# Performance work log

Hardware: AMD Instinct MI355X
Metric: run time of the kernel (lower is better)

The kernel has to match this reference:

```python
import jax, jax.numpy as jnp
import numpy as np

B, S, D = 32, 1024, 128
NUM_VT = 32
MIN_DR, MAX_DR = 0.0, 30.0
MIN_SOG, MAX_SOG = 0.0, 40.0
MIN_ROT, MAX_ROT = -127.0, 127.0


def setup_inputs() -> dict:
    key = jax.random.key(0)
    ks = jax.random.split(key, 32)
    u = lambda k, lo, hi: jax.random.uniform(k, (B, S, 1), minval=lo, maxval=hi, dtype=jnp.float32)
    lon = u(ks[0], -180.0, 180.0)
    lat = u(ks[1], -90.0, 90.0)
    rot = u(ks[2], MIN_ROT, MAX_ROT)
    sog = u(ks[3], MIN_SOG, MAX_SOG)
    cog = u(ks[4], 0.0, 360.0)
    head = u(ks[5], 0.0, 360.0)
    vtype = jax.random.randint(ks[6], (B, S, 1), 0, NUM_VT).astype(jnp.float32)
    dr = u(ks[7], MIN_DR, MAX_DR)
    ais_data = jnp.concatenate([lon, lat, rot, sog, cog, head, vtype, dr], axis=-1)
    p = lambda k, shape: (jax.random.normal(k, shape, dtype=jnp.float32) * 0.05)
    return {
        "ais_data": ais_data,
        "W_lon1": p(ks[8], (2, D)), "b_lon1": p(ks[9], (D,)),
        "W_lon2": p(ks[10], (D, D)), "b_lon2": p(ks[11], (D,)),
        "W_lat1": p(ks[12], (2, D)), "b_lat1": p(ks[13], (D,)),
        "W_lat2": p(ks[14], (D, D)), "b_lat2": p(ks[15], (D,)),
        "W_cog": p(ks[16], (2, D)), "b_cog": p(ks[17], (D,)),
        "W_head": p(ks[18], (2, D)), "b_head": p(ks[19], (D,)),
        "W_dr": p(ks[20], (1, D)), "b_dr": p(ks[21], (D,)),
        "W_sog": p(ks[22], (1, D)), "b_sog": p(ks[23], (D,)),
        "W_rot": p(ks[24], (1, D)), "b_rot": p(ks[25], (D,)),
        "emb": p(ks[26], (NUM_VT, D)),
    }


def reference(ais_data, W_lon1, b_lon1, W_lon2, b_lon2, W_lat1, b_lat1, W_lat2, b_lat2,
              W_cog, b_cog, W_head, b_head, W_dr, b_dr, W_sog, b_sog, W_rot, b_rot, emb):
    deg2rad = jnp.pi / 180.0
    lon = ais_data[..., 0:1]
    lat = ais_data[..., 1:2]
    rot = ais_data[..., 2:3]
    sog = ais_data[..., 3:4]
    cog = ais_data[..., 4:5]
    head = ais_data[..., 5:6]
    vtype = ais_data[..., 6]
    dr = ais_data[..., 7:8]

    def coord(x, mask_val, W1, b1, W2, b2):
        # x: [b,s,1] degrees -> 2-layer MLP on [sin, cos]
        xr = x * deg2rad
        f = jnp.concatenate([jnp.sin(xr), jnp.cos(xr)], axis=-1)  # [b,s,2]
        e = jax.nn.relu(f @ W1 + b1) @ W2 + b2                    # [b,s,D]
        return jnp.where(x == mask_val, 0.0, e)

    def cyclical(x, W, b):
        xr = x * deg2rad - jnp.pi
        f = jnp.concatenate([jnp.sin(xr), jnp.cos(xr)], axis=-1)
        e = f @ W + b
        return jnp.where(x == -1.0, 0.0, e)

    def continuous(x, mn, mx, W, b):
        xn = 2.0 * (x - mn) / jnp.maximum(mx - mn, 1e-6) - 1.0
        e = jnp.tanh(xn @ W + b)
        return jnp.where(x == -1.0, 0.0, e)

    enc_lon = coord(lon, 181.0, W_lon1, b_lon1, W_lon2, b_lon2)
    enc_lat = coord(lat, 91.0, W_lat1, b_lat1, W_lat2, b_lat2)
    enc_rot = continuous(rot, MIN_ROT, MAX_ROT, W_rot, b_rot)
    enc_sog = continuous(sog, MIN_SOG, MAX_SOG, W_sog, b_sog)
    enc_cog = cyclical(cog, W_cog, b_cog)
    enc_head = cyclical(head, W_head, b_head)
    vt_idx = jax.lax.stop_gradient(vtype).astype(jnp.int32)
    enc_vt = emb[vt_idx]                                          # [b,s,D]
    enc_dr = continuous(dr, MIN_DR, MAX_DR, W_dr, b_dr)

    # order matches torch.cat((spatial(lon,lat), rot, sog, cog, heading, vessel_type, draught))
    out = jnp.stack([enc_lon, enc_lat, enc_rot, enc_sog, enc_cog, enc_head, enc_vt, enc_dr], axis=2)
    b, s = ais_data.shape[:2]
    return out.reshape(b, s, -1)  # [b, s, 8*D]
```

## Files before the change

kernel.cpp:

```cpp
#include <hip/hip_runtime.h>
#include <cstdint>

typedef short bf16x8 __attribute__((ext_vector_type(8)));
typedef float f32x4 __attribute__((ext_vector_type(4)));

#define D2R 0.017453292519943295f
#define PI_F 3.14159265358979323846f

__device__ __forceinline__ unsigned bf16r(float x) {
    unsigned u = __float_as_uint(x);
    return (u + 0x7fffu + ((u >> 16) & 1u)) >> 16;
}

__device__ __forceinline__ float tanh_fast(float x) {
    float e = __expf(2.0f * x);
    return 1.0f - 2.0f / (e + 1.0f);
}

__global__ __launch_bounds__(256, 2) void hae_kernel(
    const float* __restrict__ ais,
    const float* __restrict__ Wlon1, const float* __restrict__ blon1,
    const float* __restrict__ Wlon2, const float* __restrict__ blon2,
    const float* __restrict__ Wlat1, const float* __restrict__ blat1,
    const float* __restrict__ Wlat2, const float* __restrict__ blat2,
    const float* __restrict__ Wcog,  const float* __restrict__ bcog,
    const float* __restrict__ Whead, const float* __restrict__ bhead,
    const float* __restrict__ Wdr,   const float* __restrict__ bdr,
    const float* __restrict__ Wsog,  const float* __restrict__ bsog,
    const float* __restrict__ Wrot,  const float* __restrict__ brot,
    const float* __restrict__ emb,
    float* __restrict__ out)
{
    __shared__ unsigned short hlds[2][64][128];
    __shared__ float s_sin[2][64], s_cos[2][64], s_mask[2][64];
    __shared__ float s_xn[3][64], s_mxn[3][64];
    __shared__ float s_scyc[2][64], s_ccyc[2][64], s_mcyc[2][64];
    __shared__ int   s_vt[64];

    const int t = threadIdx.x;
    const int tok0 = blockIdx.x * 64;

    if (t < 64) {
        const float* a = ais + (size_t)(tok0 + t) * 8;
        f32x4 a0 = *(const f32x4*)a;
        f32x4 a1 = *(const f32x4*)(a + 4);
        float lon = a0[0], lat = a0[1], rot = a0[2], sog = a0[3];
        float cog = a1[0], head = a1[1], vt = a1[2], dr = a1[3];

        float lr = lon * D2R;
        s_sin[0][t] = __sinf(lr); s_cos[0][t] = __cosf(lr);
        s_mask[0][t] = (lon == 181.0f) ? 0.f : 1.f;
        float tr = lat * D2R;
        s_sin[1][t] = __sinf(tr); s_cos[1][t] = __cosf(tr);
        s_mask[1][t] = (lat == 91.0f) ? 0.f : 1.f;

        s_xn[0][t] = (rot + 127.0f) * (2.0f / 254.0f) - 1.0f;
        s_mxn[0][t] = (rot == -1.0f) ? 0.f : 1.f;
        s_xn[1][t] = sog * (2.0f / 40.0f) - 1.0f;
        s_mxn[1][t] = (sog == -1.0f) ? 0.f : 1.f;
        s_xn[2][t] = dr * (2.0f / 30.0f) - 1.0f;
        s_mxn[2][t] = (dr == -1.0f) ? 0.f : 1.f;

        float cr = cog * D2R - PI_F;
        s_scyc[0][t] = __sinf(cr); s_ccyc[0][t] = __cosf(cr);
        s_mcyc[0][t] = (cog == -1.0f) ? 0.f : 1.f;
        float hr = head * D2R - PI_F;
        s_scyc[1][t] = __sinf(hr); s_ccyc[1][t] = __cosf(hr);
        s_mcyc[1][t] = (head == -1.0f) ? 0.f : 1.f;
        s_vt[t] = (int)vt;
    }
    __syncthreads();

    {
        const int jj = t & 63;
        const int j0 = jj * 2;
        const int quad = t >> 6;
        float w00a = Wlon1[j0],       w00b = Wlon1[j0 + 1];
        float w01a = Wlon1[128 + j0], w01b = Wlon1[128 + j0 + 1];
        float b0a  = blon1[j0],       b0b  = blon1[j0 + 1];
        float w10a = Wlat1[j0],       w10b = Wlat1[j0 + 1];
        float w11a = Wlat1[128 + j0], w11b = Wlat1[128 + j0 + 1];
        float b1a  = blat1[j0],       b1b  = blat1[j0 + 1];
        char* base0 = (char*)&hlds[0][0][0];
        char* base1 = (char*)&hlds[1][0][0];
        #pragma unroll
        for (int p = 0; p < 16; ++p) {
            int i = quad + p * 4;
            int sw = (j0 * 2) ^ ((i & 7) << 4);
            float s0 = s_sin[0][i], c0 = s_cos[0][i];
            float h0 = fmaxf(fmaf(s0, w00a, fmaf(c0, w01a, b0a)), 0.f);
            float h1 = fmaxf(fmaf(s0, w00b, fmaf(c0, w01b, b0b)), 0.f);
            *(unsigned*)(base0 + i * 256 + sw) = bf16r(h0) | (bf16r(h1) << 16);
            float s1 = s_sin[1][i], c1 = s_cos[1][i];
            float g0 = fmaxf(fmaf(s1, w10a, fmaf(c1, w11a, b1a)), 0.f);
            float g1 = fmaxf(fmaf(s1, w10b, fmaf(c1, w11b, b1b)), 0.f);
            *(unsigned*)(base1 + i * 256 + sw) = bf16r(g0) | (bf16r(g1) << 16);
        }
    }
    __syncthreads();

    const int w  = t >> 6;
    const int l  = t & 63;
    const int c  = w & 1;
    const int mh = w >> 1;
    const float* W2 = c ? Wlat2 : Wlon2;
    const float* b2 = c ? blat2 : blon2;
    const int col = l & 15;
    const int q   = l >> 4;

    bf16x8 afrag[2][4];
    {
        char* hb = (char*)&hlds[c][0][0];
        #pragma unroll
        for (int mt = 0; mt < 2; ++mt) {
            int row = mh * 32 + mt * 16 + col;
            #pragma unroll
            for (int ks = 0; ks < 4; ++ks) {
                int jb = (ks * 32 + q * 8) * 2;
                afrag[mt][ks] = *(bf16x8*)(hb + row * 256 + (jb ^ ((row & 7) << 4)));
            }
        }
    }

    f32x4 acc[2][8];
    #pragma unroll
    for (int mt = 0; mt < 2; ++mt)
        #pragma unroll
        for (int nt = 0; nt < 8; ++nt)
            acc[mt][nt] = (f32x4){0.f, 0.f, 0.f, 0.f};

    #pragma unroll
    for (int nt = 0; nt < 8; ++nt) {
        const int d = nt * 16 + col;
        bf16x8 bfrag[4];
        #pragma unroll
        for (int ks = 0; ks < 4; ++ks) {
            int kb = ks * 32 + q * 8;
            bf16x8 bf;
            #pragma unroll
            for (int e = 0; e < 8; ++e)
                bf[e] = (short)bf16r(W2[(size_t)(kb + e) * 128 + d]);
            bfrag[ks] = bf;
        }
        #pragma unroll
        for (int mt = 0; mt < 2; ++mt)
            #pragma unroll
            for (int ks = 0; ks < 4; ++ks)
                acc[mt][nt] = __builtin_amdgcn_mfma_f32_16x16x32_bf16(
                    afrag[mt][ks], bfrag[ks], acc[mt][nt], 0, 0, 0);
    }

    #pragma unroll
    for (int nt = 0; nt < 8; ++nt) {
        int d = nt * 16 + col;
        float bb = b2[d];
        #pragma unroll
        for (int mt = 0; mt < 2; ++mt) {
            int tokb = mh * 32 + mt * 16 + q * 4;
            #pragma unroll
            for (int r = 0; r < 4; ++r) {
                int tl = tokb + r;
                float v = (acc[mt][nt][r] + bb) * s_mask[c][tl];
                out[(size_t)(tok0 + tl) * 1024 + c * 128 + d] = v;
            }
        }
    }

    {
        const int d4 = (t & 31) * 4;
        const int io = t >> 5;
        f32x4 wr  = *(const f32x4*)(Wrot + d4),        br_ = *(const f32x4*)(brot + d4);
        f32x4 wsg = *(const f32x4*)(Wsog + d4),        bs_ = *(const f32x4*)(bsog + d4);
        f32x4 wdd = *(const f32x4*)(Wdr + d4),         bd_ = *(const f32x4*)(bdr + d4);
        f32x4 wc0 = *(const f32x4*)(Wcog + d4),  wc1 = *(const f32x4*)(Wcog + 128 + d4),  bc_ = *(const f32x4*)(bcog + d4);
        f32x4 wh0 = *(const f32x4*)(Whead + d4), wh1 = *(const f32x4*)(Whead + 128 + d4), bh_ = *(const f32x4*)(bhead + d4);
        #pragma unroll
        for (int p = 0; p < 8; ++p) {
            int i = io + p * 8;
            float* ob = out + (size_t)(tok0 + i) * 1024;
            {
                float xn = s_xn[0][i], mk = s_mxn[0][i];
                f32x4 v;
                #pragma unroll
                for (int e = 0; e < 4; ++e) v[e] = tanh_fast(fmaf(xn, wr[e], br_[e])) * mk;
                *(f32x4*)(ob + 2 * 128 + d4) = v;
            }
            {
                float xn = s_xn[1][i], mk = s_mxn[1][i];
                f32x4 v;
                #pragma unroll
                for (int e = 0; e < 4; ++e) v[e] = tanh_fast(fmaf(xn, wsg[e], bs_[e])) * mk;
                *(f32x4*)(ob + 3 * 128 + d4) = v;
            }
            {
                float sc = s_scyc[0][i], cc = s_ccyc[0][i], mk = s_mcyc[0][i];
                f32x4 v;
                #pragma unroll
                for (int e = 0; e < 4; ++e) v[e] = fmaf(sc, wc0[e], fmaf(cc, wc1[e], bc_[e])) * mk;
                *(f32x4*)(ob + 4 * 128 + d4) = v;
            }
            {
                float sc = s_scyc[1][i], cc = s_ccyc[1][i], mk = s_mcyc[1][i];
                f32x4 v;
                #pragma unroll
                for (int e = 0; e < 4; ++e) v[e] = fmaf(sc, wh0[e], fmaf(cc, wh1[e], bh_[e])) * mk;
                *(f32x4*)(ob + 5 * 128 + d4) = v;
            }
            {
                f32x4 ev = *(const f32x4*)(emb + (size_t)s_vt[i] * 128 + d4);
                *(f32x4*)(ob + 6 * 128 + d4) = ev;
            }
            {
                float xn = s_xn[2][i], mk = s_mxn[2][i];
                f32x4 v;
                #pragma unroll
                for (int e = 0; e < 4; ++e) v[e] = tanh_fast(fmaf(xn, wdd[e], bd_[e])) * mk;
                *(f32x4*)(ob + 7 * 128 + d4) = v;
            }
        }
    }
}

extern "C" void kernel_launch(void* const* d_in, const int* in_sizes, int n_in,
                              void* d_out, int out_size, void* d_ws, size_t ws_size,
                              hipStream_t stream) {
    (void)in_sizes; (void)n_in; (void)d_ws; (void)ws_size; (void)out_size;
    const float* ais   = (const float*)d_in[0];
    const float* Wlon1 = (const float*)d_in[1];
    const float* blon1 = (const float*)d_in[2];
    const float* Wlon2 = (const float*)d_in[3];
    const float* blon2 = (const float*)d_in[4];
    const float* Wlat1 = (const float*)d_in[5];
    const float* blat1 = (const float*)d_in[6];
    const float* Wlat2 = (const float*)d_in[7];
    const float* blat2 = (const float*)d_in[8];
    const float* Wcog  = (const float*)d_in[9];
    const float* bcog  = (const float*)d_in[10];
    const float* Whead = (const float*)d_in[11];
    const float* bhead = (const float*)d_in[12];
    const float* Wdr   = (const float*)d_in[13];
    const float* bdr   = (const float*)d_in[14];
    const float* Wsog  = (const float*)d_in[15];
    const float* bsog  = (const float*)d_in[16];
    const float* Wrot  = (const float*)d_in[17];
    const float* brot  = (const float*)d_in[18];
    const float* emb   = (const float*)d_in[19];
    float* out = (float*)d_out;

    hae_kernel<<<512, 256, 0, stream>>>(ais,
        Wlon1, blon1, Wlon2, blon2,
        Wlat1, blat1, Wlat2, blat2,
        Wcog, bcog, Whead, bhead,
        Wdr, bdr, Wsog, bsog, Wrot, brot,
        emb, out);
}
```

Before: 34.22 us.

## Pretranspose W2 to bf16 in a prep kernel and halve tokens per block

Adds a prep kernel that converts Wlon2/Wlat2 to bf16 in a transposed [d][k] workspace layout, so the main kernel loads B fragments as 16-byte vectors instead of doing eight strided scalar loads plus conversion per fragment. Blocks now handle 32 tokens instead of 64, doubling the grid and raising the occupancy hint to 4. The elementwise encoder stores are moved ahead of the MFMA stage so they overlap with it. The cost is an extra kernel launch and workspace traffic on every call.

Result: slower. 40.62 us (+18.7%).

```diff
diff --git a/kernel.cpp b/kernel.cpp
--- a/kernel.cpp
+++ b/kernel.cpp
@@ -17,30 +17,44 @@
     return 1.0f - 2.0f / (e + 1.0f);
 }
 
-__global__ __launch_bounds__(256, 2) void hae_kernel(
+__global__ void prep_w2(const float* __restrict__ Wlon2,
+                        const float* __restrict__ Wlat2,
+                        unsigned short* __restrict__ w2t) {
+    int idx = blockIdx.x * 256 + threadIdx.x;
+    if (idx < 32768) {
+        int c = idx >> 14;
+        int r = idx & 16383;
+        int d = r >> 7, k = r & 127;
+        const float* W = c ? Wlat2 : Wlon2;
+        w2t[idx] = (unsigned short)bf16r(W[(size_t)k * 128 + d]);
+    }
+}
+
+__global__ __launch_bounds__(256, 4) void hae_kernel(
     const float* __restrict__ ais,
     const float* __restrict__ Wlon1, const float* __restrict__ blon1,
-    const float* __restrict__ Wlon2, const float* __restrict__ blon2,
+    const float* __restrict__ blon2,
     const float* __restrict__ Wlat1, const float* __restrict__ blat1,
-    const float* __restrict__ Wlat2, const float* __restrict__ blat2,
+    const float* __restrict__ blat2,
     const float* __restrict__ Wcog,  const float* __restrict__ bcog,
     const float* __restrict__ Whead, const float* __restrict__ bhead,
     const float* __restrict__ Wdr,   const float* __restrict__ bdr,
     const float* __restrict__ Wsog,  const float* __restrict__ bsog,
     const float* __restrict__ Wrot,  const float* __restrict__ brot,
     const float* __restrict__ emb,
+    const unsigned short* __restrict__ w2t,
     float* __restrict__ out)
 {
-    __shared__ unsigned short hlds[2][64][128];
-    __shared__ float s_sin[2][64], s_cos[2][64], s_mask[2][64];
-    __shared__ float s_xn[3][64], s_mxn[3][64];
-    __shared__ float s_scyc[2][64], s_ccyc[2][64], s_mcyc[2][64];
-    __shared__ int   s_vt[64];
+    __shared__ unsigned short hlds[2][32][128];
+    __shared__ float s_sin[2][32], s_cos[2][32], s_mask[2][32];
+    __shared__ float s_xn[3][32], s_mxn[3][32];
+    __shared__ float s_scyc[2][32], s_ccyc[2][32], s_mcyc[2][32];
+    __shared__ int   s_vt[32];
 
     const int t = threadIdx.x;
-    const int tok0 = blockIdx.x * 64;
-
-    if (t < 64) {
+    const int tok0 = blockIdx.x * 32;
+
+    if (t < 32) {
         const float* a = ais + (size_t)(tok0 + t) * 8;
         f32x4 a0 = *(const f32x4*)a;
         f32x4 a1 = *(const f32x4*)(a + 4);
@@ -72,8 +86,7 @@
     __syncthreads();
 
     {
-        const int jj = t & 63;
-        const int j0 = jj * 2;
+        const int j0 = (t & 63) * 2;
         const int quad = t >> 6;
         float w00a = Wlon1[j0],       w00b = Wlon1[j0 + 1];
         float w01a = Wlon1[128 + j0], w01b = Wlon1[128 + j0 + 1];
@@ -84,7 +97,7 @@
         char* base0 = (char*)&hlds[0][0][0];
         char* base1 = (char*)&hlds[1][0][0];
         #pragma unroll
-        for (int p = 0; p < 16; ++p) {
+        for (int p = 0; p < 8; ++p) {
             int i = quad + p * 4;
             int sw = (j0 * 2) ^ ((i & 7) << 4);
             float s0 = s_sin[0][i], c0 = s_cos[0][i];
@@ -97,74 +110,6 @@
             *(unsigned*)(base1 + i * 256 + sw) = bf16r(g0) | (bf16r(g1) << 16);
         }
     }
-    __syncthreads();
-
-    const int w  = t >> 6;
-    const int l  = t & 63;
-    const int c  = w & 1;
-    const int mh = w >> 1;
-    const float* W2 = c ? Wlat2 : Wlon2;
-    const float* b2 = c ? blat2 : blon2;
-    const int col = l & 15;
-    const int q   = l >> 4;
-
-    bf16x8 afrag[2][4];
-    {
-        char* hb = (char*)&hlds[c][0][0];
-        #pragma unroll
-        for (int mt = 0; mt < 2; ++mt) {
-            int row = mh * 32 + mt * 16 + col;
-            #pragma unroll
-            for (int ks = 0; ks < 4; ++ks) {
-                int jb = (ks * 32 + q * 8) * 2;
-                afrag[mt][ks] = *(bf16x8*)(hb + row * 256 + (jb ^ ((row & 7) << 4)));
-            }
-        }
-    }
-
-    f32x4 acc[2][8];
-    #pragma unroll
-    for (int mt = 0; mt < 2; ++mt)
-        #pragma unroll
-        for (int nt = 0; nt < 8; ++nt)
-            acc[mt][nt] = (f32x4){0.f, 0.f, 0.f, 0.f};
-
-    #pragma unroll
-    for (int nt = 0; nt < 8; ++nt) {
-        const int d = nt * 16 + col;
-        bf16x8 bfrag[4];
-        #pragma unroll
-        for (int ks = 0; ks < 4; ++ks) {
-            int kb = ks * 32 + q * 8;
-            bf16x8 bf;
-            #pragma unroll
-            for (int e = 0; e < 8; ++e)
-                bf[e] = (short)bf16r(W2[(size_t)(kb + e) * 128 + d]);
-            bfrag[ks] = bf;
-        }
-        #pragma unroll
-        for (int mt = 0; mt < 2; ++mt)
-            #pragma unroll
-            for (int ks = 0; ks < 4; ++ks)
-                acc[mt][nt] = __builtin_amdgcn_mfma_f32_16x16x32_bf16(
-                    afrag[mt][ks], bfrag[ks], acc[mt][nt], 0, 0, 0);
-    }
-
-    #pragma unroll
-    for (int nt = 0; nt < 8; ++nt) {
-        int d = nt * 16 + col;
-        float bb = b2[d];
-        #pragma unroll
-        for (int mt = 0; mt < 2; ++mt) {
-            int tokb = mh * 32 + mt * 16 + q * 4;
-            #pragma unroll
-            for (int r = 0; r < 4; ++r) {
-                int tl = tokb + r;
-                float v = (acc[mt][nt][r] + bb) * s_mask[c][tl];
-                out[(size_t)(tok0 + tl) * 1024 + c * 128 + d] = v;
-            }
-        }
-    }
 
     {
         const int d4 = (t & 31) * 4;
@@ -175,7 +120,7 @@
         f32x4 wc0 = *(const f32x4*)(Wcog + d4),  wc1 = *(const f32x4*)(Wcog + 128 + d4),  bc_ = *(const f32x4*)(bcog + d4);
         f32x4 wh0 = *(const f32x4*)(Whead + d4), wh1 = *(const f32x4*)(Whead + 128 + d4), bh_ = *(const f32x4*)(bhead + d4);
         #pragma unroll
-        for (int p = 0; p < 8; ++p) {
+        for (int p = 0; p < 4; ++p) {
             int i = io + p * 8;
             float* ob = out + (size_t)(tok0 + i) * 1024;
             {
@@ -218,13 +163,60 @@
                 *(f32x4*)(ob + 7 * 128 + d4) = v;
             }
         }
+    }
+    __syncthreads();
+
+    const int w  = t >> 6;
+    const int l  = t & 63;
+    const int c  = w & 1;
+    const int mh = w >> 1;
+    const float* b2 = c ? blat2 : blon2;
+    const int col = l & 15;
+    const int q   = l >> 4;
+
+    bf16x8 afrag[4];
+    {
+        char* hb = (char*)&hlds[c][0][0];
+        int row = mh * 16 + col;
+        int swr = (row & 7) << 4;
+        #pragma unroll
+        for (int ks = 0; ks < 4; ++ks) {
+            int jb = (ks * 32 + q * 8) * 2;
+            afrag[ks] = *(bf16x8*)(hb + row * 256 + (jb ^ swr));
+        }
+    }
+
+    float msk[4];
+    #pragma unroll
+    for (int r = 0; r < 4; ++r) msk[r] = s_mask[c][mh * 16 + q * 4 + r];
+
+    const unsigned short* w2tc = w2t + c * 16384;
+    const size_t obase = (size_t)(tok0 + mh * 16 + q * 4) * 1024 + c * 128;
+
+    #pragma unroll
+    for (int nt = 0; nt < 8; ++nt) {
+        const int d = nt * 16 + col;
+        const unsigned short* wp = w2tc + d * 128 + q * 8;
+        bf16x8 b0 = *(const bf16x8*)(wp);
+        bf16x8 b1 = *(const bf16x8*)(wp + 32);
+        bf16x8 b2f = *(const bf16x8*)(wp + 64);
+        bf16x8 b3 = *(const bf16x8*)(wp + 96);
+        f32x4 acc = (f32x4){0.f, 0.f, 0.f, 0.f};
+        acc = __builtin_amdgcn_mfma_f32_16x16x32_bf16(afrag[0], b0,  acc, 0, 0, 0);
+        acc = __builtin_amdgcn_mfma_f32_16x16x32_bf16(afrag[1], b1,  acc, 0, 0, 0);
+        acc = __builtin_amdgcn_mfma_f32_16x16x32_bf16(afrag[2], b2f, acc, 0, 0, 0);
+        acc = __builtin_amdgcn_mfma_f32_16x16x32_bf16(afrag[3], b3,  acc, 0, 0, 0);
+        float bb = b2[d];
+        #pragma unroll
+        for (int r = 0; r < 4; ++r)
+            out[obase + (size_t)r * 1024 + d] = (acc[r] + bb) * msk[r];
     }
 }
 
 extern "C" void kernel_launch(void* const* d_in, const int* in_sizes, int n_in,
                               void* d_out, int out_size, void* d_ws, size_t ws_size,
                               hipStream_t stream) {
-    (void)in_sizes; (void)n_in; (void)d_ws; (void)ws_size; (void)out_size;
+    (void)in_sizes; (void)n_in; (void)ws_size; (void)out_size;
     const float* ais   = (const float*)d_in[0];
     const float* Wlon1 = (const float*)d_in[1];
     const float* blon1 = (const float*)d_in[2];
@@ -246,11 +238,13 @@
     const float* brot  = (const float*)d_in[18];
     const float* emb   = (const float*)d_in[19];
     float* out = (float*)d_out;
-
-    hae_kernel<<<512, 256, 0, stream>>>(ais,
-        Wlon1, blon1, Wlon2, blon2,
-        Wlat1, blat1, Wlat2, blat2,
+    unsigned short* w2t = (unsigned short*)d_ws;
+
+    prep_w2<<<128, 256, 0, stream>>>(Wlon2, Wlat2, w2t);
+    hae_kernel<<<1024, 256, 0, stream>>>(ais,
+        Wlon1, blon1, blon2,
+        Wlat1, blat1, blat2,
         Wcog, bcog, Whead, bhead,
         Wdr, bdr, Wsog, bsog, Wrot, brot,
-        emb, out);
-}
+        emb, w2t, out);
+}
```

## Move MFMA stage after elementwise encoders and split GEMM work by output columns

Applied to the files above, without the earlier changes.

The coordinate-MLP second-layer GEMM now runs after the elementwise encoders, and the barrier before it is moved. The B-fragment weight loads and conversion are hoisted before that barrier, so the global weight fetches overlap the wait for the hidden-layer LDS writes. Work is also repartitioned: each wave now covers all 64 tokens for half the output columns instead of half the tokens for all columns. This lowers the live accumulator count to one f32x4 at a time, with stores issued per tile. The trade-off is more register pressure from the 16 held B fragments, and a different store pattern.

After: 29.34 us. 14.3% less time.

```diff
diff --git a/kernel.cpp b/kernel.cpp
--- a/kernel.cpp
+++ b/kernel.cpp
@@ -72,8 +72,7 @@
     __syncthreads();
 
     {
-        const int jj = t & 63;
-        const int j0 = jj * 2;
+        const int j0 = (t & 63) * 2;
         const int quad = t >> 6;
         float w00a = Wlon1[j0],       w00b = Wlon1[j0 + 1];
         float w01a = Wlon1[128 + j0], w01b = Wlon1[128 + j0 + 1];
@@ -97,74 +96,6 @@
             *(unsigned*)(base1 + i * 256 + sw) = bf16r(g0) | (bf16r(g1) << 16);
         }
     }
-    __syncthreads();
-
-    const int w  = t >> 6;
-    const int l  = t & 63;
-    const int c  = w & 1;
-    const int mh = w >> 1;
-    const float* W2 = c ? Wlat2 : Wlon2;
-    const float* b2 = c ? blat2 : blon2;
-    const int col = l & 15;
-    const int q   = l >> 4;
-
-    bf16x8 afrag[2][4];
-    {
-        char* hb = (char*)&hlds[c][0][0];
-        #pragma unroll
-        for (int mt = 0; mt < 2; ++mt) {
-            int row = mh * 32 + mt * 16 + col;
-            #pragma unroll
-            for (int ks = 0; ks < 4; ++ks) {
-                int jb = (ks * 32 + q * 8) * 2;
-                afrag[mt][ks] = *(bf16x8*)(hb + row * 256 + (jb ^ ((row & 7) << 4)));
-            }
-        }
-    }
-
-    f32x4 acc[2][8];
-    #pragma unroll
-    for (int mt = 0; mt < 2; ++mt)
-        #pragma unroll
-        for (int nt = 0; nt < 8; ++nt)
-            acc[mt][nt] = (f32x4){0.f, 0.f, 0.f, 0.f};
-
-    #pragma unroll
-    for (int nt = 0; nt < 8; ++nt) {
-        const int d = nt * 16 + col;
-        bf16x8 bfrag[4];
-        #pragma unroll
-        for (int ks = 0; ks < 4; ++ks) {
-            int kb = ks * 32 + q * 8;
-            bf16x8 bf;
-            #pragma unroll
-            for (int e = 0; e < 8; ++e)
-                bf[e] = (short)bf16r(W2[(size_t)(kb + e) * 128 + d]);
-            bfrag[ks] = bf;
-        }
-        #pragma unroll
-        for (int mt = 0; mt < 2; ++mt)
-            #pragma unroll
-            for (int ks = 0; ks < 4; ++ks)
-                acc[mt][nt] = __builtin_amdgcn_mfma_f32_16x16x32_bf16(
-                    afrag[mt][ks], bfrag[ks], acc[mt][nt], 0, 0, 0);
-    }
-
-    #pragma unroll
-    for (int nt = 0; nt < 8; ++nt) {
-        int d = nt * 16 + col;
-        float bb = b2[d];
-        #pragma unroll
-        for (int mt = 0; mt < 2; ++mt) {
-            int tokb = mh * 32 + mt * 16 + q * 4;
-            #pragma unroll
-            for (int r = 0; r < 4; ++r) {
-                int tl = tokb + r;
-                float v = (acc[mt][nt][r] + bb) * s_mask[c][tl];
-                out[(size_t)(tok0 + tl) * 1024 + c * 128 + d] = v;
-            }
-        }
-    }
 
     {
         const int d4 = (t & 31) * 4;
@@ -217,6 +148,62 @@
                 for (int e = 0; e < 4; ++e) v[e] = tanh_fast(fmaf(xn, wdd[e], bd_[e])) * mk;
                 *(f32x4*)(ob + 7 * 128 + d4) = v;
             }
+        }
+    }
+
+    const int w  = t >> 6;
+    const int l  = t & 63;
+    const int c  = w & 1;
+    const int nh = w >> 1;
+    const float* W2  = c ? Wlat2 : Wlon2;
+    const float* b2p = c ? blat2 : blon2;
+    const int col = l & 15;
+    const int q   = l >> 4;
+
+    bf16x8 bfrag[4][4];
+    float  bb[4];
+    #pragma unroll
+    for (int nt = 0; nt < 4; ++nt) {
+        const int d = nh * 64 + nt * 16 + col;
+        bb[nt] = b2p[d];
+        #pragma unroll
+        for (int ks = 0; ks < 4; ++ks) {
+            const int kb = ks * 32 + q * 8;
+            bf16x8 bf;
+            #pragma unroll
+            for (int e = 0; e < 8; ++e)
+                bf[e] = (short)bf16r(W2[(size_t)(kb + e) * 128 + d]);
+            bfrag[nt][ks] = bf;
+        }
+    }
+    __syncthreads();
+
+    char* hb = (char*)&hlds[c][0][0];
+    #pragma unroll
+    for (int mt = 0; mt < 4; ++mt) {
+        const int row = mt * 16 + col;
+        const int swr = (row & 7) << 4;
+        bf16x8 afrag[4];
+        #pragma unroll
+        for (int ks = 0; ks < 4; ++ks) {
+            int jb = (ks * 32 + q * 8) * 2;
+            afrag[ks] = *(bf16x8*)(hb + row * 256 + (jb ^ swr));
+        }
+        float msk[4];
+        #pragma unroll
+        for (int r = 0; r < 4; ++r) msk[r] = s_mask[c][mt * 16 + q * 4 + r];
+        const size_t obase = (size_t)(tok0 + mt * 16 + q * 4) * 1024 + c * 128 + nh * 64;
+
+        #pragma unroll
+        for (int nt = 0; nt < 4; ++nt) {
+            f32x4 acc = (f32x4){0.f, 0.f, 0.f, 0.f};
+            acc = __builtin_amdgcn_mfma_f32_16x16x32_bf16(afrag[0], bfrag[nt][0], acc, 0, 0, 0);
+            acc = __builtin_amdgcn_mfma_f32_16x16x32_bf16(afrag[1], bfrag[nt][1], acc, 0, 0, 0);
+            acc = __builtin_amdgcn_mfma_f32_16x16x32_bf16(afrag[2], bfrag[nt][2], acc, 0, 0, 0);
+            acc = __builtin_amdgcn_mfma_f32_16x16x32_bf16(afrag[3], bfrag[nt][3], acc, 0, 0, 0);
+            #pragma unroll
+            for (int r = 0; r < 4; ++r)
+                out[obase + (size_t)r * 1024 + nt * 16 + col] = (acc[r] + bb[nt]) * msk[r];
         }
     }
 }
```
